# Optimization experiments

Hardware: AMD Instinct MI355X
Metric: run time of the kernel (lower is better)

Reference implementation:

```python
import jax, jax.numpy as jnp
import numpy as np

N_NODES = 100000


def sage_conv(x, src, dst, W_l, b_l, W_r):
    # PyG SAGEConv (aggr='mean'): out = lin_l(mean_j x_j) + lin_r(x_i)
    msg = x[src]  # [E, d] gather of source-node features
    agg = jax.ops.segment_sum(msg, dst, num_segments=N_NODES)  # [N, d]
    deg = jax.ops.segment_sum(jnp.ones((src.shape[0],), x.dtype), dst,
                              num_segments=N_NODES)
    mean = agg / jnp.clip(deg, 1.0, None)[:, None]
    return mean @ W_l.T + b_l + x @ W_r.T


def setup_inputs() -> dict:
    key = jax.random.key(0)
    ks = jax.random.split(key, 12)
    d_in, d_h, d_out, n_edges = 64, 64, 2, 1200000
    s = 1.0 / np.sqrt(d_h)
    inp = {
        "x": jax.random.normal(ks[0], (N_NODES, d_in), dtype=jnp.float32),
        "edge_index": jax.random.randint(ks[1], (2, n_edges), 0, N_NODES,
                                         dtype=jnp.int64),
        "W_l1": jax.random.uniform(ks[2], (d_h, d_in), jnp.float32, -s, s),
        "b_l1": jax.random.uniform(ks[3], (d_h,), jnp.float32, -s, s),
        "W_r1": jax.random.uniform(ks[4], (d_h, d_in), jnp.float32, -s, s),
        "W_l2": jax.random.uniform(ks[5], (d_h, d_h), jnp.float32, -s, s),
        "b_l2": jax.random.uniform(ks[6], (d_h,), jnp.float32, -s, s),
        "W_r2": jax.random.uniform(ks[7], (d_h, d_h), jnp.float32, -s, s),
        "W_c": jax.random.uniform(ks[8], (d_out, d_h), jnp.float32, -s, s),
        "b_c": jax.random.uniform(ks[9], (d_out,), jnp.float32, -s, s),
    }
    return inp


def reference(x, edge_index, W_l1, b_l1, W_r1, W_l2, b_l2, W_r2, W_c, b_c):
    src, dst = edge_index[0], edge_index[1]
    # layer 1 + relu (dropout is identity in eval mode)
    h = jax.nn.relu(sage_conv(x, src, dst, W_l1, b_l1, W_r1))
    # layer 2 (no relu per forward())
    h = sage_conv(h, src, dst, W_l2, b_l2, W_r2)
    # classifier
    return h @ W_c.T + b_c
```

## Files before the change

### kernel.cpp

```cpp
#include <hip/hip_runtime.h>

#define N_NODES 100000
#define D 64
#define NBUCK 391
#define NBLK_A 512
#define GCNT_N (NBUCK * NBLK_A)
#define NCHUNK ((GCNT_N + 255) / 256)
#define NTILE (N_NODES / 32)

typedef __attribute__((ext_vector_type(8))) short short8;
typedef __attribute__((ext_vector_type(16))) float f32x16;
union Pack8 { uint4 u; short8 s; };

__device__ __forceinline__ unsigned f2bf(float f) {
  unsigned u = __float_as_uint(f);
  return (u + 0x7fffu + ((u >> 16) & 1u)) >> 16;
}
#define BF_LO(u) __uint_as_float(((unsigned)(u)) << 16)
#define BF_HI(u) __uint_as_float(((unsigned)(u)) & 0xffff0000u)


__global__ __launch_bounds__(256) void passA_count(const int* __restrict__ dst,
                                                   int* __restrict__ gcnt,
                                                   int nE, int ec) {
  __shared__ int cnt[NBUCK];
  int t = threadIdx.x, blk = blockIdx.x;
  for (int i = t; i < NBUCK; i += 256) cnt[i] = 0;
  __syncthreads();
  int e0 = blk * ec, e1 = min(e0 + ec, nE);
  for (int e = e0 + t; e < e1; e += 256) atomicAdd(&cnt[dst[e] >> 8], 1);
  __syncthreads();
  for (int b = t; b < NBUCK; b += 256) gcnt[b * NBLK_A + blk] = cnt[b];
}

__global__ void gscan_p1(const int* __restrict__ g, int* __restrict__ csum) {
  int t = threadIdx.x, b = blockIdx.x;
  int i = b * 256 + t;
  int v = (i < GCNT_N) ? g[i] : 0;
  for (int off = 32; off; off >>= 1) v += __shfl_down(v, off);
  __shared__ int ws4[4];
  if ((t & 63) == 0) ws4[t >> 6] = v;
  __syncthreads();
  if (t == 0) csum[b] = ws4[0] + ws4[1] + ws4[2] + ws4[3];
}

__global__ void gscan_p2(int* __restrict__ csum, int nB) {
  __shared__ int s[1024];
  int t = threadIdx.x;
  int orig = (t < nB) ? csum[t] : 0;
  s[t] = orig;
  __syncthreads();
  for (int off = 1; off < 1024; off <<= 1) {
    int v = (t >= off) ? s[t - off] : 0;
    __syncthreads();
    s[t] += v;
    __syncthreads();
  }
  if (t < nB) csum[t] = s[t] - orig;
}

__global__ void gscan_p3(int* __restrict__ g, const int* __restrict__ csum) {
  __shared__ int s[256];
  int t = threadIdx.x, b = blockIdx.x;
  int i = b * 256 + t;
  int d = (i < GCNT_N) ? g[i] : 0;
  s[t] = d;
  __syncthreads();
  for (int off = 1; off < 256; off <<= 1) {
    int v = (t >= off) ? s[t - off] : 0;
    __syncthreads();
    s[t] += v;
    __syncthreads();
  }
  if (i < GCNT_N) g[i] = s[t] - d + csum[b];
}

__global__ __launch_bounds__(256) void passC_place(const int* __restrict__ src,
                                                   const int* __restrict__ dst,
                                                   const int* __restrict__ S,
                                                   uint2* __restrict__ pairs,
                                                   int nE, int ec) {
  __shared__ int cur[NBUCK];
  int t = threadIdx.x, blk = blockIdx.x;
  for (int b = t; b < NBUCK; b += 256) cur[b] = S[b * NBLK_A + blk];
  __syncthreads();
  int e0 = blk * ec, e1 = min(e0 + ec, nE);
  for (int e = e0 + t; e < e1; e += 256) {
    int d = dst[e];
    int p = atomicAdd(&cur[d >> 8], 1);
    pairs[p] = make_uint2((unsigned)d, (unsigned)src[e]);
  }
}

__global__ __launch_bounds__(256) void passD_csr(const uint2* __restrict__ pairs,
                                                 const int* __restrict__ S,
                                                 int* __restrict__ rowstart,
                                                 int* __restrict__ degI,
                                                 int* __restrict__ adj, int nE) {
  __shared__ int lh[256];
  __shared__ int sc[256];
  __shared__ int cur[256];
  int t = threadIdx.x, b = blockIdx.x;
  int base = S[b * NBLK_A];
  int end = (b == NBUCK - 1) ? nE : S[(b + 1) * NBLK_A];
  lh[t] = 0;
  __syncthreads();
  for (int p = base + t; p < end; p += 256) atomicAdd(&lh[pairs[p].x & 255], 1);
  __syncthreads();
  int d = lh[t];
  sc[t] = d;
  __syncthreads();
  for (int off = 1; off < 256; off <<= 1) {
    int v = (t >= off) ? sc[t - off] : 0;
    __syncthreads();
    sc[t] += v;
    __syncthreads();
  }
  int ex = sc[t] - d;
  int node = b * 256 + t;
  if (node < N_NODES) {
    rowstart[node] = base + ex;
    degI[node] = d;
  }
  cur[t] = base + ex;
  __syncthreads();
  for (int p = base + t; p < end; p += 256) {
    uint2 e = pairs[p];
    int slot = atomicAdd(&cur[e.x & 255], 1);
    adj[slot] = (int)e.y;
  }
}

__global__ void wfold_kernel(const float* __restrict__ Wc,
                             const float* __restrict__ Wl2,
                             const float* __restrict__ Wr2,
                             const float* __restrict__ bl2,
                             const float* __restrict__ bc,
                             float* __restrict__ A2, float* __restrict__ B2,
                             float* __restrict__ bfv) {
  int t = threadIdx.x;
  int c = t >> 6, k = t & 63;
  float sa = 0.f, sb = 0.f;
  for (int j = 0; j < 64; ++j) {
    float w = Wc[c * 64 + j];
    sa = fmaf(w, Wl2[j * 64 + k], sa);
    sb = fmaf(w, Wr2[j * 64 + k], sb);
  }
  A2[c * 64 + k] = sa;
  B2[c * 64 + k] = sb;
  if (t < 2) {
    float s = bc[t];
    for (int j = 0; j < 64; ++j) s = fmaf(Wc[t * 64 + j], bl2[j], s);
    bfv[t] = s;
  }
}

__global__ void wprep_kernel(const float* __restrict__ Wl,
                             const float* __restrict__ Wr,
                             unsigned short* __restrict__ wcat) {
  int i = blockIdx.x * 256 + threadIdx.x;
  if (i < 4096) wcat[i] = (unsigned short)f2bf(Wl[i]);
  else if (i < 8192) wcat[i] = (unsigned short)f2bf(Wr[i - 4096]);
}

__global__ __launch_bounds__(256) void transform_mfma(
    const float* __restrict__ x, const unsigned short* __restrict__ wcat,
    const float* __restrict__ bl, unsigned short* __restrict__ t1,
    float* __restrict__ r1) {
  int tid = threadIdx.x, lane = tid & 63;
  int l31 = lane & 31, hi = lane >> 5;

  short8 af[4][4];
#pragma unroll
  for (int jt = 0; jt < 4; ++jt)
#pragma unroll
    for (int kk = 0; kk < 4; ++kk)
      af[jt][kk] = *(const short8*)(wcat + (jt * 32 + l31) * 64 + kk * 16 + 8 * hi);

  const f32x16 Z = {0.f, 0.f, 0.f, 0.f, 0.f, 0.f, 0.f, 0.f,
                    0.f, 0.f, 0.f, 0.f, 0.f, 0.f, 0.f, 0.f};
  const float4* x4 = (const float4*)x;

  int gw = (blockIdx.x * 256 + tid) >> 6;
  int nW = (gridDim.x * 256) >> 6;

  for (int tile = gw; tile < NTILE; tile += nW) {
    int base = tile * 32;
    int node = base + l31;
    f32x16 acc[4] = {Z, Z, Z, Z};
#pragma unroll
    for (int kk = 0; kk < 4; ++kk) {
      float4 fa = x4[(size_t)node * 16 + kk * 4 + 2 * hi];
      float4 fb = x4[(size_t)node * 16 + kk * 4 + 2 * hi + 1];
      Pack8 pk;
      pk.u.x = f2bf(fa.x) | (f2bf(fa.y) << 16);
      pk.u.y = f2bf(fa.z) | (f2bf(fa.w) << 16);
      pk.u.z = f2bf(fb.x) | (f2bf(fb.y) << 16);
      pk.u.w = f2bf(fb.z) | (f2bf(fb.w) << 16);
      acc[0] = __builtin_amdgcn_mfma_f32_32x32x16_bf16(af[0][kk], pk.s, acc[0], 0, 0, 0);
      acc[1] = __builtin_amdgcn_mfma_f32_32x32x16_bf16(af[1][kk], pk.s, acc[1], 0, 0, 0);
      acc[2] = __builtin_amdgcn_mfma_f32_32x32x16_bf16(af[2][kk], pk.s, acc[2], 0, 0, 0);
      acc[3] = __builtin_amdgcn_mfma_f32_32x32x16_bf16(af[3][kk], pk.s, acc[3], 0, 0, 0);
    }
#pragma unroll
    for (int jt = 0; jt < 2; ++jt)
#pragma unroll
      for (int rg = 0; rg < 4; ++rg) {
        int j0 = jt * 32 + 8 * rg + 4 * hi;
        uint2 p;
        p.x = f2bf(acc[jt][4 * rg + 0]) | (f2bf(acc[jt][4 * rg + 1]) << 16);
        p.y = f2bf(acc[jt][4 * rg + 2]) | (f2bf(acc[jt][4 * rg + 3]) << 16);
        *(uint2*)(t1 + (size_t)node * 64 + j0) = p;
      }
#pragma unroll
    for (int jt = 2; jt < 4; ++jt)
#pragma unroll
      for (int rg = 0; rg < 4; ++rg) {
        int j0 = (jt - 2) * 32 + 8 * rg + 4 * hi;
        float4 bv = ((const float4*)bl)[j0 >> 2];
        float4 o;
        o.x = acc[jt][4 * rg + 0] + bv.x;
        o.y = acc[jt][4 * rg + 1] + bv.y;
        o.z = acc[jt][4 * rg + 2] + bv.z;
        o.w = acc[jt][4 * rg + 3] + bv.w;
        *(float4*)(r1 + (size_t)node * 64 + j0) = o;
      }
  }
}

#define ACC8(v, m)                       \
  acc[0] = fmaf(BF_LO(v.x), m, acc[0]);  \
  acc[1] = fmaf(BF_HI(v.x), m, acc[1]);  \
  acc[2] = fmaf(BF_LO(v.y), m, acc[2]);  \
  acc[3] = fmaf(BF_HI(v.y), m, acc[3]);  \
  acc[4] = fmaf(BF_LO(v.z), m, acc[4]);  \
  acc[5] = fmaf(BF_HI(v.z), m, acc[5]);  \
  acc[6] = fmaf(BF_LO(v.w), m, acc[6]);  \
  acc[7] = fmaf(BF_HI(v.w), m, acc[7]);

__global__ __launch_bounds__(512) void gather1_kernel(
    const int* __restrict__ rowstart, const int* __restrict__ degI,
    const int* __restrict__ adj, const unsigned short* __restrict__ t1,
    const float* __restrict__ r1, const float* __restrict__ A2,
    const float* __restrict__ B2, float2* __restrict__ g2,
    float2* __restrict__ s2, int nE) {
  int tid = threadIdx.x, lane = tid & 63;
  int o = lane >> 3, j8 = lane & 7;
  float pa0[8], pa1[8], pb0[8], pb1[8];
  {
    float4 a = ((const float4*)A2)[j8 * 2], b = ((const float4*)A2)[j8 * 2 + 1];
    pa0[0] = a.x; pa0[1] = a.y; pa0[2] = a.z; pa0[3] = a.w;
    pa0[4] = b.x; pa0[5] = b.y; pa0[6] = b.z; pa0[7] = b.w;
    a = ((const float4*)A2)[16 + j8 * 2]; b = ((const float4*)A2)[16 + j8 * 2 + 1];
    pa1[0] = a.x; pa1[1] = a.y; pa1[2] = a.z; pa1[3] = a.w;
    pa1[4] = b.x; pa1[5] = b.y; pa1[6] = b.z; pa1[7] = b.w;
    a = ((const float4*)B2)[j8 * 2]; b = ((const float4*)B2)[j8 * 2 + 1];
    pb0[0] = a.x; pb0[1] = a.y; pb0[2] = a.z; pb0[3] = a.w;
    pb0[4] = b.x; pb0[5] = b.y; pb0[6] = b.z; pb0[7] = b.w;
    a = ((const float4*)B2)[16 + j8 * 2]; b = ((const float4*)B2)[16 + j8 * 2 + 1];
    pb1[0] = a.x; pb1[1] = a.y; pb1[2] = a.z; pb1[3] = a.w;
    pb1[4] = b.x; pb1[5] = b.y; pb1[6] = b.z; pb1[7] = b.w;
  }

  int gw = (blockIdx.x * 512 + tid) >> 6;
  int nWaves = (gridDim.x * 512) >> 6;

  for (int n = gw; n < N_NODES; n += nWaves) {
    int rs = rowstart[n], dg = degI[n];
    float acc[8] = {0.f, 0.f, 0.f, 0.f, 0.f, 0.f, 0.f, 0.f};
    for (int base = 0; base < dg; base += 64) {
      int cnt = min(dg - base, 64);
      int a = adj[min(rs + base + lane, nE - 1)];
      for (int t = 0; t < cnt; t += 16) {
        int el0 = t + o, el1 = t + 8 + o;
        int nb0 = __shfl(a, el0);
        int nb1 = __shfl(a, el1);
        bool ok0 = el0 < cnt, ok1 = el1 < cnt;
        nb0 = ok0 ? nb0 : n;
        nb1 = ok1 ? nb1 : n;
        uint4 v0 = *(const uint4*)(t1 + (size_t)nb0 * 64 + j8 * 8);
        uint4 v1 = *(const uint4*)(t1 + (size_t)nb1 * 64 + j8 * 8);
        float m0 = ok0 ? 1.f : 0.f, m1 = ok1 ? 1.f : 0.f;
        ACC8(v0, m0)
        ACC8(v1, m1)
      }
    }
#pragma unroll
    for (int jj = 0; jj < 8; ++jj) {
      acc[jj] += __shfl_xor(acc[jj], 8);
      acc[jj] += __shfl_xor(acc[jj], 16);
      acc[jj] += __shfl_xor(acc[jj], 32);
    }
    float inv = 1.f / (float)max(dg, 1);
    float4 ra = ((const float4*)r1)[(size_t)n * 16 + j8 * 2];
    float4 rb = ((const float4*)r1)[(size_t)n * 16 + j8 * 2 + 1];
    float h[8];
    h[0] = fmaxf(fmaf(acc[0], inv, ra.x), 0.f);
    h[1] = fmaxf(fmaf(acc[1], inv, ra.y), 0.f);
    h[2] = fmaxf(fmaf(acc[2], inv, ra.z), 0.f);
    h[3] = fmaxf(fmaf(acc[3], inv, ra.w), 0.f);
    h[4] = fmaxf(fmaf(acc[4], inv, rb.x), 0.f);
    h[5] = fmaxf(fmaf(acc[5], inv, rb.y), 0.f);
    h[6] = fmaxf(fmaf(acc[6], inv, rb.z), 0.f);
    h[7] = fmaxf(fmaf(acc[7], inv, rb.w), 0.f);
    float d0 = 0.f, d1 = 0.f, d2 = 0.f, d3 = 0.f;
#pragma unroll
    for (int i = 0; i < 8; ++i) {
      d0 = fmaf(h[i], pa0[i], d0);
      d1 = fmaf(h[i], pa1[i], d1);
      d2 = fmaf(h[i], pb0[i], d2);
      d3 = fmaf(h[i], pb1[i], d3);
    }
    d0 += __shfl_xor(d0, 1); d0 += __shfl_xor(d0, 2); d0 += __shfl_xor(d0, 4);
    d1 += __shfl_xor(d1, 1); d1 += __shfl_xor(d1, 2); d1 += __shfl_xor(d1, 4);
    d2 += __shfl_xor(d2, 1); d2 += __shfl_xor(d2, 2); d2 += __shfl_xor(d2, 4);
    d3 += __shfl_xor(d3, 1); d3 += __shfl_xor(d3, 2); d3 += __shfl_xor(d3, 4);
    if (lane == 0) {
      g2[n] = make_float2(d0, d1);
      s2[n] = make_float2(d2, d3);
    }
  }
}

__global__ __launch_bounds__(256) void gather2_kernel(
    const int* __restrict__ rowstart, const int* __restrict__ degI,
    const int* __restrict__ adj, const float2* __restrict__ g2,
    const float2* __restrict__ s2, const float* __restrict__ bfv,
    float* __restrict__ out, int nE) {
  int tid = threadIdx.x, lane = tid & 63;
  int q = lane >> 4, l16 = lane & 15;
  float bf0 = bfv[0], bf1 = bfv[1];
  int gq = ((blockIdx.x * 256 + tid) >> 6) * 4 + q;
  int strideN = ((gridDim.x * 256) >> 6) * 4;
  for (int n = gq; n < N_NODES; n += strideN) {
    int rs = rowstart[n], dg = degI[n];
    float s0 = 0.f, s1 = 0.f;
    for (int base = 0; base < dg; base += 16) {
      int e = base + l16;
      int a = adj[min(rs + e, nE - 1)];
      float2 v = g2[a];
      float m = (e < dg) ? 1.f : 0.f;
      s0 = fmaf(v.x, m, s0);
      s1 = fmaf(v.y, m, s1);
    }
    s0 += __shfl_xor(s0, 1); s0 += __shfl_xor(s0, 2);
    s0 += __shfl_xor(s0, 4); s0 += __shfl_xor(s0, 8);
    s1 += __shfl_xor(s1, 1); s1 += __shfl_xor(s1, 2);
    s1 += __shfl_xor(s1, 4); s1 += __shfl_xor(s1, 8);
    if (l16 == 0) {
      float inv = 1.f / (float)max(dg, 1);
      float2 sv = s2[n];
      out[(size_t)n * 2 + 0] = fmaf(s0, inv, sv.x) + bf0;
      out[(size_t)n * 2 + 1] = fmaf(s1, inv, sv.y) + bf1;
    }
  }
}

extern "C" void kernel_launch(void* const* d_in, const int* in_sizes, int n_in,
                              void* d_out, int out_size, void* d_ws,
                              size_t ws_size, hipStream_t stream) {
  const float* x   = (const float*)d_in[0];
  const int*   ei  = (const int*)d_in[1];
  const float* Wl1 = (const float*)d_in[2];
  const float* bl1 = (const float*)d_in[3];
  const float* Wr1 = (const float*)d_in[4];
  const float* Wl2 = (const float*)d_in[5];
  const float* bl2 = (const float*)d_in[6];
  const float* Wr2 = (const float*)d_in[7];
  const float* Wc  = (const float*)d_in[8];
  const float* bc  = (const float*)d_in[9];
  float* out = (float*)d_out;

  int nE = in_sizes[1] / 2;
  const int* src = ei;
  const int* dst = ei + nE;

  float* r1 = (float*)d_ws;
  uint2* pairs = (uint2*)d_ws;
  unsigned short* t1 = (unsigned short*)(r1 + (size_t)N_NODES * D);
  float2* g2 = (float2*)(t1 + (size_t)N_NODES * D);
  float2* s2 = g2 + N_NODES;
  float* A2 = (float*)(s2 + N_NODES);
  float* B2 = A2 + 128;
  float* bfv = B2 + 128;
  unsigned short* wcat = (unsigned short*)(bfv + 4);
  int* degI = (int*)(wcat + 8192);
  int* rowstart = degI + N_NODES;
  int* gcnt = rowstart + N_NODES;
  int* csum = gcnt + GCNT_N;
  int* adj = csum + 1024;

  int ec = (nE + NBLK_A - 1) / NBLK_A;

  passA_count<<<NBLK_A, 256, 0, stream>>>(dst, gcnt, nE, ec);
  gscan_p1<<<NCHUNK, 256, 0, stream>>>(gcnt, csum);
  gscan_p2<<<1, 1024, 0, stream>>>(csum, NCHUNK);
  gscan_p3<<<NCHUNK, 256, 0, stream>>>(gcnt, csum);
  passC_place<<<NBLK_A, 256, 0, stream>>>(src, dst, gcnt, pairs, nE, ec);
  passD_csr<<<NBUCK, 256, 0, stream>>>(pairs, gcnt, rowstart, degI, adj, nE);

  wfold_kernel<<<1, 128, 0, stream>>>(Wc, Wl2, Wr2, bl2, bc, A2, B2, bfv);
  wprep_kernel<<<32, 256, 0, stream>>>(Wl1, Wr1, wcat);
  transform_mfma<<<512, 256, 0, stream>>>(x, wcat, bl1, t1, r1);
  gather1_kernel<<<1024, 512, 0, stream>>>(rowstart, degI, adj, t1, r1, A2,
                                           B2, g2, s2, nE);
  gather2_kernel<<<512, 256, 0, stream>>>(rowstart, degI, adj, g2, s2, bfv,
                                          out, nE);
}
```

Measured before the change: 149.0 us.

## Store root term in bf16 and process two nodes per wave in gather1

The root-linear output r1 is now written and read as bf16 instead of fp32, which halves that intermediate's traffic. gather1 now handles two destination nodes per wave so more independent gather loads are in flight, and the folded weight vectors move from per-lane registers into shared memory. Out-of-range adjacency reads now fall back to a valid index. The cost is extra rounding error on the root term and wasted masked loads when the two paired nodes have very different degrees.

Measured after the change: 145.7 us. 1.02x faster.

```diff
diff --git a/kernel.cpp b/kernel.cpp
--- a/kernel.cpp
+++ b/kernel.cpp
@@ -166,7 +166,7 @@
 __global__ __launch_bounds__(256) void transform_mfma(
     const float* __restrict__ x, const unsigned short* __restrict__ wcat,
     const float* __restrict__ bl, unsigned short* __restrict__ t1,
-    float* __restrict__ r1) {
+    unsigned short* __restrict__ r1b) {
   int tid = threadIdx.x, lane = tid & 63;
   int l31 = lane & 31, hi = lane >> 5;
 
@@ -185,8 +185,7 @@
   int nW = (gridDim.x * 256) >> 6;
 
   for (int tile = gw; tile < NTILE; tile += nW) {
-    int base = tile * 32;
-    int node = base + l31;
+    int node = tile * 32 + l31;
     f32x16 acc[4] = {Z, Z, Z, Z};
 #pragma unroll
     for (int kk = 0; kk < 4; ++kk) {
@@ -218,106 +217,120 @@
       for (int rg = 0; rg < 4; ++rg) {
         int j0 = (jt - 2) * 32 + 8 * rg + 4 * hi;
         float4 bv = ((const float4*)bl)[j0 >> 2];
-        float4 o;
-        o.x = acc[jt][4 * rg + 0] + bv.x;
-        o.y = acc[jt][4 * rg + 1] + bv.y;
-        o.z = acc[jt][4 * rg + 2] + bv.z;
-        o.w = acc[jt][4 * rg + 3] + bv.w;
-        *(float4*)(r1 + (size_t)node * 64 + j0) = o;
+        uint2 p;
+        p.x = f2bf(acc[jt][4 * rg + 0] + bv.x) |
+              (f2bf(acc[jt][4 * rg + 1] + bv.y) << 16);
+        p.y = f2bf(acc[jt][4 * rg + 2] + bv.z) |
+              (f2bf(acc[jt][4 * rg + 3] + bv.w) << 16);
+        *(uint2*)(r1b + (size_t)node * 64 + j0) = p;
       }
   }
 }
 
-#define ACC8(v, m)                       \
-  acc[0] = fmaf(BF_LO(v.x), m, acc[0]);  \
-  acc[1] = fmaf(BF_HI(v.x), m, acc[1]);  \
-  acc[2] = fmaf(BF_LO(v.y), m, acc[2]);  \
-  acc[3] = fmaf(BF_HI(v.y), m, acc[3]);  \
-  acc[4] = fmaf(BF_LO(v.z), m, acc[4]);  \
-  acc[5] = fmaf(BF_HI(v.z), m, acc[5]);  \
-  acc[6] = fmaf(BF_LO(v.w), m, acc[6]);  \
+#define ACC8(acc, v, m)                     \
+  acc[0] = fmaf(BF_LO(v.x), m, acc[0]);     \
+  acc[1] = fmaf(BF_HI(v.x), m, acc[1]);     \
+  acc[2] = fmaf(BF_LO(v.y), m, acc[2]);     \
+  acc[3] = fmaf(BF_HI(v.y), m, acc[3]);     \
+  acc[4] = fmaf(BF_LO(v.z), m, acc[4]);     \
+  acc[5] = fmaf(BF_HI(v.z), m, acc[5]);     \
+  acc[6] = fmaf(BF_LO(v.w), m, acc[6]);     \
   acc[7] = fmaf(BF_HI(v.w), m, acc[7]);
 
 __global__ __launch_bounds__(512) void gather1_kernel(
     const int* __restrict__ rowstart, const int* __restrict__ degI,
     const int* __restrict__ adj, const unsigned short* __restrict__ t1,
-    const float* __restrict__ r1, const float* __restrict__ A2,
+    const unsigned short* __restrict__ r1b, const float* __restrict__ A2,
     const float* __restrict__ B2, float2* __restrict__ g2,
     float2* __restrict__ s2, int nE) {
-  int tid = threadIdx.x, lane = tid & 63;
+  __shared__ float pAB[4][64];
+  int tid = threadIdx.x;
+  if (tid < 256) {
+    int v = tid >> 6, f = tid & 63;
+    pAB[v][f] = (v < 2) ? A2[v * 64 + f] : B2[(v - 2) * 64 + f];
+  }
+  __syncthreads();
+
+  int lane = tid & 63;
   int o = lane >> 3, j8 = lane & 7;
-  float pa0[8], pa1[8], pb0[8], pb1[8];
-  {
-    float4 a = ((const float4*)A2)[j8 * 2], b = ((const float4*)A2)[j8 * 2 + 1];
-    pa0[0] = a.x; pa0[1] = a.y; pa0[2] = a.z; pa0[3] = a.w;
-    pa0[4] = b.x; pa0[5] = b.y; pa0[6] = b.z; pa0[7] = b.w;
-    a = ((const float4*)A2)[16 + j8 * 2]; b = ((const float4*)A2)[16 + j8 * 2 + 1];
-    pa1[0] = a.x; pa1[1] = a.y; pa1[2] = a.z; pa1[3] = a.w;
-    pa1[4] = b.x; pa1[5] = b.y; pa1[6] = b.z; pa1[7] = b.w;
-    a = ((const float4*)B2)[j8 * 2]; b = ((const float4*)B2)[j8 * 2 + 1];
-    pb0[0] = a.x; pb0[1] = a.y; pb0[2] = a.z; pb0[3] = a.w;
-    pb0[4] = b.x; pb0[5] = b.y; pb0[6] = b.z; pb0[7] = b.w;
-    a = ((const float4*)B2)[16 + j8 * 2]; b = ((const float4*)B2)[16 + j8 * 2 + 1];
-    pb1[0] = a.x; pb1[1] = a.y; pb1[2] = a.z; pb1[3] = a.w;
-    pb1[4] = b.x; pb1[5] = b.y; pb1[6] = b.z; pb1[7] = b.w;
-  }
-
   int gw = (blockIdx.x * 512 + tid) >> 6;
-  int nWaves = (gridDim.x * 512) >> 6;
-
-  for (int n = gw; n < N_NODES; n += nWaves) {
-    int rs = rowstart[n], dg = degI[n];
-    float acc[8] = {0.f, 0.f, 0.f, 0.f, 0.f, 0.f, 0.f, 0.f};
-    for (int base = 0; base < dg; base += 64) {
-      int cnt = min(dg - base, 64);
-      int a = adj[min(rs + base + lane, nE - 1)];
-      for (int t = 0; t < cnt; t += 16) {
+  int nW = (gridDim.x * 512) >> 6;
+
+  for (int n = gw * 2; n < N_NODES; n += nW * 2) {
+    int n1 = n + 1;
+    int rs0 = rowstart[n], dg0 = degI[n];
+    int rs1 = rowstart[n1], dg1 = degI[n1];
+    float acc0[8] = {0.f, 0.f, 0.f, 0.f, 0.f, 0.f, 0.f, 0.f};
+    float acc1[8] = {0.f, 0.f, 0.f, 0.f, 0.f, 0.f, 0.f, 0.f};
+    int mx = max(dg0, dg1);
+    for (int base = 0; base < mx; base += 64) {
+      int cnt0 = min(max(dg0 - base, 0), 64);
+      int cnt1 = min(max(dg1 - base, 0), 64);
+      int a0 = adj[min(rs0 + base + ((lane < cnt0) ? lane : 0), nE - 1)];
+      int a1 = adj[min(rs1 + base + ((lane < cnt1) ? lane : 0), nE - 1)];
+      int mc = max(cnt0, cnt1);
+      for (int t = 0; t < mc; t += 16) {
         int el0 = t + o, el1 = t + 8 + o;
-        int nb0 = __shfl(a, el0);
-        int nb1 = __shfl(a, el1);
-        bool ok0 = el0 < cnt, ok1 = el1 < cnt;
-        nb0 = ok0 ? nb0 : n;
-        nb1 = ok1 ? nb1 : n;
-        uint4 v0 = *(const uint4*)(t1 + (size_t)nb0 * 64 + j8 * 8);
-        uint4 v1 = *(const uint4*)(t1 + (size_t)nb1 * 64 + j8 * 8);
-        float m0 = ok0 ? 1.f : 0.f, m1 = ok1 ? 1.f : 0.f;
-        ACC8(v0, m0)
-        ACC8(v1, m1)
+        int b00 = __shfl(a0, el0), b01 = __shfl(a0, el1);
+        int b10 = __shfl(a1, el0), b11 = __shfl(a1, el1);
+        bool k00 = el0 < cnt0, k01 = el1 < cnt0;
+        bool k10 = el0 < cnt1, k11 = el1 < cnt1;
+        b00 = k00 ? b00 : n;  b01 = k01 ? b01 : n;
+        b10 = k10 ? b10 : n1; b11 = k11 ? b11 : n1;
+        uint4 v00 = *(const uint4*)(t1 + (size_t)b00 * 64 + j8 * 8);
+        uint4 v01 = *(const uint4*)(t1 + (size_t)b01 * 64 + j8 * 8);
+        uint4 v10 = *(const uint4*)(t1 + (size_t)b10 * 64 + j8 * 8);
+        uint4 v11 = *(const uint4*)(t1 + (size_t)b11 * 64 + j8 * 8);
+        float m00 = k00 ? 1.f : 0.f, m01 = k01 ? 1.f : 0.f;
+        float m10 = k10 ? 1.f : 0.f, m11 = k11 ? 1.f : 0.f;
+        ACC8(acc0, v00, m00)
+        ACC8(acc0, v01, m01)
+        ACC8(acc1, v10, m10)
+        ACC8(acc1, v11, m11)
       }
     }
 #pragma unroll
     for (int jj = 0; jj < 8; ++jj) {
-      acc[jj] += __shfl_xor(acc[jj], 8);
-      acc[jj] += __shfl_xor(acc[jj], 16);
-      acc[jj] += __shfl_xor(acc[jj], 32);
-    }
-    float inv = 1.f / (float)max(dg, 1);
-    float4 ra = ((const float4*)r1)[(size_t)n * 16 + j8 * 2];
-    float4 rb = ((const float4*)r1)[(size_t)n * 16 + j8 * 2 + 1];
-    float h[8];
-    h[0] = fmaxf(fmaf(acc[0], inv, ra.x), 0.f);
-    h[1] = fmaxf(fmaf(acc[1], inv, ra.y), 0.f);
-    h[2] = fmaxf(fmaf(acc[2], inv, ra.z), 0.f);
-    h[3] = fmaxf(fmaf(acc[3], inv, ra.w), 0.f);
-    h[4] = fmaxf(fmaf(acc[4], inv, rb.x), 0.f);
-    h[5] = fmaxf(fmaf(acc[5], inv, rb.y), 0.f);
-    h[6] = fmaxf(fmaf(acc[6], inv, rb.z), 0.f);
-    h[7] = fmaxf(fmaf(acc[7], inv, rb.w), 0.f);
-    float d0 = 0.f, d1 = 0.f, d2 = 0.f, d3 = 0.f;
-#pragma unroll
-    for (int i = 0; i < 8; ++i) {
-      d0 = fmaf(h[i], pa0[i], d0);
-      d1 = fmaf(h[i], pa1[i], d1);
-      d2 = fmaf(h[i], pb0[i], d2);
-      d3 = fmaf(h[i], pb1[i], d3);
-    }
-    d0 += __shfl_xor(d0, 1); d0 += __shfl_xor(d0, 2); d0 += __shfl_xor(d0, 4);
-    d1 += __shfl_xor(d1, 1); d1 += __shfl_xor(d1, 2); d1 += __shfl_xor(d1, 4);
-    d2 += __shfl_xor(d2, 1); d2 += __shfl_xor(d2, 2); d2 += __shfl_xor(d2, 4);
-    d3 += __shfl_xor(d3, 1); d3 += __shfl_xor(d3, 2); d3 += __shfl_xor(d3, 4);
-    if (lane == 0) {
-      g2[n] = make_float2(d0, d1);
-      s2[n] = make_float2(d2, d3);
+      acc0[jj] += __shfl_xor(acc0[jj], 8);
+      acc0[jj] += __shfl_xor(acc0[jj], 16);
+      acc0[jj] += __shfl_xor(acc0[jj], 32);
+      acc1[jj] += __shfl_xor(acc1[jj], 8);
+      acc1[jj] += __shfl_xor(acc1[jj], 16);
+      acc1[jj] += __shfl_xor(acc1[jj], 32);
+    }
+#pragma unroll
+    for (int nn = 0; nn < 2; ++nn) {
+      int nd = nn ? n1 : n;
+      float* acc = nn ? acc1 : acc0;
+      int dg = nn ? dg1 : dg0;
+      float inv = 1.f / (float)max(dg, 1);
+      uint4 rv = *(const uint4*)(r1b + (size_t)nd * 64 + j8 * 8);
+      float h[8];
+      h[0] = fmaxf(fmaf(acc[0], inv, BF_LO(rv.x)), 0.f);
+      h[1] = fmaxf(fmaf(acc[1], inv, BF_HI(rv.x)), 0.f);
+      h[2] = fmaxf(fmaf(acc[2], inv, BF_LO(rv.y)), 0.f);
+      h[3] = fmaxf(fmaf(acc[3], inv, BF_HI(rv.y)), 0.f);
+      h[4] = fmaxf(fmaf(acc[4], inv, BF_LO(rv.z)), 0.f);
+      h[5] = fmaxf(fmaf(acc[5], inv, BF_HI(rv.z)), 0.f);
+      h[6] = fmaxf(fmaf(acc[6], inv, BF_LO(rv.w)), 0.f);
+      h[7] = fmaxf(fmaf(acc[7], inv, BF_HI(rv.w)), 0.f);
+      float d0 = 0.f, d1 = 0.f, d2 = 0.f, d3 = 0.f;
+#pragma unroll
+      for (int i = 0; i < 8; ++i) {
+        float hv = h[i];
+        d0 = fmaf(hv, pAB[0][j8 * 8 + i], d0);
+        d1 = fmaf(hv, pAB[1][j8 * 8 + i], d1);
+        d2 = fmaf(hv, pAB[2][j8 * 8 + i], d2);
+        d3 = fmaf(hv, pAB[3][j8 * 8 + i], d3);
+      }
+      d0 += __shfl_xor(d0, 1); d0 += __shfl_xor(d0, 2); d0 += __shfl_xor(d0, 4);
+      d1 += __shfl_xor(d1, 1); d1 += __shfl_xor(d1, 2); d1 += __shfl_xor(d1, 4);
+      d2 += __shfl_xor(d2, 1); d2 += __shfl_xor(d2, 2); d2 += __shfl_xor(d2, 4);
+      d3 += __shfl_xor(d3, 1); d3 += __shfl_xor(d3, 2); d3 += __shfl_xor(d3, 4);
+      if (lane == 0) {
+        g2[nd] = make_float2(d0, d1);
+        s2[nd] = make_float2(d2, d3);
+      }
     }
   }
 }
@@ -337,7 +350,7 @@
     float s0 = 0.f, s1 = 0.f;
     for (int base = 0; base < dg; base += 16) {
       int e = base + l16;
-      int a = adj[min(rs + e, nE - 1)];
+      int a = adj[min(rs + ((e < dg) ? e : 0), nE - 1)];
       float2 v = g2[a];
       float m = (e < dg) ? 1.f : 0.f;
       s0 = fmaf(v.x, m, s0);
@@ -375,9 +388,9 @@
   const int* src = ei;
   const int* dst = ei + nE;
 
-  float* r1 = (float*)d_ws;
+  unsigned short* r1b = (unsigned short*)d_ws;
   uint2* pairs = (uint2*)d_ws;
-  unsigned short* t1 = (unsigned short*)(r1 + (size_t)N_NODES * D);
+  unsigned short* t1 = r1b + (size_t)N_NODES * D;
   float2* g2 = (float2*)(t1 + (size_t)N_NODES * D);
   float2* s2 = g2 + N_NODES;
   float* A2 = (float*)(s2 + N_NODES);
@@ -401,8 +414,8 @@
 
   wfold_kernel<<<1, 128, 0, stream>>>(Wc, Wl2, Wr2, bl2, bc, A2, B2, bfv);
   wprep_kernel<<<32, 256, 0, stream>>>(Wl1, Wr1, wcat);
-  transform_mfma<<<512, 256, 0, stream>>>(x, wcat, bl1, t1, r1);
-  gather1_kernel<<<1024, 512, 0, stream>>>(rowstart, degI, adj, t1, r1, A2,
+  transform_mfma<<<512, 256, 0, stream>>>(x, wcat, bl1, t1, r1b);
+  gather1_kernel<<<1024, 512, 0, stream>>>(rowstart, degI, adj, t1, r1b, A2,
                                            B2, g2, s2, nE);
   gather2_kernel<<<512, 256, 0, stream>>>(rowstart, degI, adj, g2, s2, bfv,
                                           out, nE);
```
